# Kernel optimization log

Measured on AMD Instinct MI355X. Metric: run time of the kernel, lower is better.

## Reference

```python
import jax, jax.numpy as jnp
import numpy as np

ALPHA = 0.9   # synaptic decay
BETA = 0.8    # membrane decay
THRESH = 1.0  # snntorch default threshold, reset_mechanism='subtract'
DIMS = [7200, 3600, 1800, 900, 450]
B, T, IN_DIM, K = 128, 16, 14400, 25


def setup_inputs() -> dict:
    key = jax.random.key(0)
    ks = jax.random.split(key, 24)
    inp = {}
    inp["x"] = jax.random.normal(ks[0], (B, T, IN_DIM), jnp.float32)
    prev = IN_DIM
    for i, d in enumerate(DIMS):
        inp[f"w{i}"] = jax.random.normal(ks[1 + i], (d, K), jnp.float32) * (2.0 / K) ** 0.5
        inp[f"b{i}"] = jax.random.normal(ks[7 + i], (d,), jnp.float32) * 0.01
        inp[f"knn{i}"] = jax.random.randint(ks[13 + i], (d, K), 0, prev)
        prev = d
    inp["fc_w"] = jax.random.normal(ks[20], (2, DIMS[-1]), jnp.float32) * 0.05
    inp["fc_b"] = jax.random.normal(ks[21], (2,), jnp.float32) * 0.01
    return inp


def _forward(x, ws, bs, knns, fc_w, fc_b):
    n_layer = len(DIMS)

    def lif(inp, syn, mem):
        # snntorch Synaptic, reset_mechanism='subtract': reset computed from
        # the PREVIOUS membrane potential and detached from the graph.
        reset = jax.lax.stop_gradient((mem > THRESH).astype(inp.dtype))
        syn = ALPHA * syn + inp
        mem = BETA * mem + syn - reset * THRESH
        return syn, mem

    def step(carry, xt):
        syns, mems = carry
        h = xt  # (B, prev_dim)
        new_syns, new_mems = [], []
        for i in range(n_layer):
            g = jnp.take(h, knns[i], axis=1)                 # (B, d_i, K) KNN gather
            pre = jnp.einsum('bdk,dk->bd', g, ws[i]) + bs[i]  # weighted sum over K
            syn, mem = lif(pre, syns[i], mems[i])
            new_syns.append(syn)
            new_mems.append(mem)
            h = mem  # module propagates membrane potential to next layer
        angle = h @ fc_w.T + fc_b  # (B, 2)
        return (tuple(new_syns), tuple(new_mems)), angle

    bsz = x.shape[0]
    syns0 = tuple(jnp.zeros((bsz, d), x.dtype) for d in DIMS)
    mems0 = tuple(jnp.zeros((bsz, d), x.dtype) for d in DIMS)
    _, angles = jax.lax.scan(step, (syns0, mems0), jnp.transpose(x, (1, 0, 2)))
    return angles[-1]  # only the final timestep's angle is returned


def reference(x, w0, w1, w2, w3, w4, b0, b1, b2, b3, b4,
              knn0, knn1, knn2, knn3, knn4, fc_w, fc_b):
    return _forward(x, (w0, w1, w2, w3, w4), (b0, b1, b2, b3, b4),
                    (knn0, knn1, knn2, knn3, knn4), fc_w, fc_b)
```

## Files before the change

kernel.cpp:

```cpp
#include <hip/hip_runtime.h>

#define ALPHA 0.9f
#define BETA  0.8f
#define K     25
#define B     128
#define T     16
#define IN_DIM 14400
#define NSL   8
#define SW    16
#define CF    96
#define NCH   150

using u16 = unsigned short;

static __device__ __forceinline__ u16 f2bf(float f) {
  union { float f; unsigned u; } c; c.f = f;
  const unsigned r = c.u + 0x7FFFu + ((c.u >> 16) & 1u);
  return (u16)(r >> 16);
}
static __device__ __forceinline__ float bf2f(u16 h) {
  union { unsigned u; float f; } c; c.u = ((unsigned)h) << 16;
  return c.f;
}

__global__ __launch_bounds__(256, 4) void transpose_pair_pinned(
    const float* __restrict__ x, u16* __restrict__ xTh, int t0, int slots) {
  __shared__ float lds[CF][33];
  const int e    = blockIdx.x & 7;
  const int slot = blockIdx.x >> 3;
  const int tid  = threadIdx.x;
  const int rid  = tid >> 3;
  const int fq   = tid & 7;
  const int tpar = rid >> 4;
  const int bl   = rid & 15;
  const int b    = e * 16 + bl;

  const int ntiles = 4 * NCH;
  for (int ti = slot; ti < ntiles; ti += slots) {
    const int tp = ti / NCH;
    const int ch = ti - tp * NCH;
    const int i0 = ch * CF;
    const int t  = t0 + tp * 2 + tpar;
    const float* xr = x + ((size_t)b * T + t) * IN_DIM + i0;
#pragma unroll
    for (int pf = 0; pf < CF / 32; ++pf) {
      const float4 v = *(const float4*)&xr[pf * 32 + fq * 4];
      lds[pf * 32 + fq * 4 + 0][rid] = v.x;
      lds[pf * 32 + fq * 4 + 1][rid] = v.y;
      lds[pf * 32 + fq * 4 + 2][rid] = v.z;
      lds[pf * 32 + fq * 4 + 3][rid] = v.w;
    }
    __syncthreads();
#pragma unroll
    for (int wp = 0; wp < CF / 32; ++wp) {
      const int f = wp * 32 + rid;
      ushort4 ov;
      ov.x = f2bf(lds[f][fq * 4 + 0]);
      ov.y = f2bf(lds[f][fq * 4 + 1]);
      ov.z = f2bf(lds[f][fq * 4 + 2]);
      ov.w = f2bf(lds[f][fq * 4 + 3]);
      *(ushort4*)&xTh[(((size_t)tp * NSL + e) * IN_DIM + (i0 + f)) * 32 +
                      fq * 4] = ov;
    }
    __syncthreads();
  }
}

template <int NTP, int NPASS>
__global__ __launch_bounds__(256, 4) void lcn_pair_bf(
    const u16* __restrict__ hsrc, const float* __restrict__ w,
    const float* __restrict__ bias, const int* __restrict__ knn,
    u16* __restrict__ memout, float* __restrict__ state,
    int dim, int dprev, int nblk, int load_state, int save_state) {
  const int e    = blockIdx.x & 7;
  const int blk  = blockIdx.x >> 3;
  const int nl   = threadIdx.x >> 3;
  const int l8   = threadIdx.x & 7;
  const int half = l8 >> 2;
  const int bq   = (l8 & 3) * 4;

#pragma unroll 1
  for (int p = 0; p < NPASS; ++p) {
    const int dd = (blk + p * nblk) * 32 + nl;
    const bool act = dd < dim;
    const int d = act ? dd : dim - 1;

    int   idx[K];
    float wr[K];
#pragma unroll
    for (int k = 0; k < K; ++k) {
      idx[k] = knn[d * K + k] * 32 + half * SW + bq;
      wr[k]  = w[d * K + k];
    }
    const float bi = bias[d];

    float4 s = make_float4(0.f, 0.f, 0.f, 0.f);
    float4 m = make_float4(0.f, 0.f, 0.f, 0.f);
    if (load_state) {
      const size_t so = ((size_t)e * dim + d) * SW + bq;
      s = *(const float4*)&state[so];
      m = *(const float4*)&state[(size_t)NSL * dim * SW + so];
    }

    for (int tp = 0; tp < NTP; ++tp) {
      const u16* hp = hsrc + ((size_t)tp * NSL + e) * dprev * 32;
      ushort4 hv[13], hw[12];
#pragma unroll
      for (int j = 0; j < 13; ++j)
        hv[j] = *(const ushort4*)&hp[idx[j]];
#pragma unroll
      for (int j = 0; j < 12; ++j)
        hw[j] = *(const ushort4*)&hp[idx[13 + j]];
      float4 a0 = make_float4(bi, bi, bi, bi);
      float4 a1 = make_float4(0.f, 0.f, 0.f, 0.f);
#pragma unroll
      for (int j = 0; j < 13; ++j) {
        const float wk = wr[j];
        if (j & 1) {
          a1.x = fmaf(wk, bf2f(hv[j].x), a1.x);
          a1.y = fmaf(wk, bf2f(hv[j].y), a1.y);
          a1.z = fmaf(wk, bf2f(hv[j].z), a1.z);
          a1.w = fmaf(wk, bf2f(hv[j].w), a1.w);
        } else {
          a0.x = fmaf(wk, bf2f(hv[j].x), a0.x);
          a0.y = fmaf(wk, bf2f(hv[j].y), a0.y);
          a0.z = fmaf(wk, bf2f(hv[j].z), a0.z);
          a0.w = fmaf(wk, bf2f(hv[j].w), a0.w);
        }
      }
#pragma unroll
      for (int j = 0; j < 12; ++j) {
        const float wk = wr[13 + j];
        if (j & 1) {
          a1.x = fmaf(wk, bf2f(hw[j].x), a1.x);
          a1.y = fmaf(wk, bf2f(hw[j].y), a1.y);
          a1.z = fmaf(wk, bf2f(hw[j].z), a1.z);
          a1.w = fmaf(wk, bf2f(hw[j].w), a1.w);
        } else {
          a0.x = fmaf(wk, bf2f(hw[j].x), a0.x);
          a0.y = fmaf(wk, bf2f(hw[j].y), a0.y);
          a0.z = fmaf(wk, bf2f(hw[j].z), a0.z);
          a0.w = fmaf(wk, bf2f(hw[j].w), a0.w);
        }
      }
      float4 acc;
      acc.x = a0.x + a1.x;
      acc.y = a0.y + a1.y;
      acc.z = a0.z + a1.z;
      acc.w = a0.w + a1.w;
      float4 oth;
      oth.x = __shfl_xor(acc.x, 4, 64);
      oth.y = __shfl_xor(acc.y, 4, 64);
      oth.z = __shfl_xor(acc.z, 4, 64);
      oth.w = __shfl_xor(acc.w, 4, 64);
      const float4 pre0 = half ? oth : acc;
      const float4 pre1 = half ? acc : oth;
      s.x = ALPHA * s.x + pre0.x;
      s.y = ALPHA * s.y + pre0.y;
      s.z = ALPHA * s.z + pre0.z;
      s.w = ALPHA * s.w + pre0.w;
      float4 meven;
      meven.x = BETA * m.x + s.x - ((m.x > 1.0f) ? 1.0f : 0.0f);
      meven.y = BETA * m.y + s.y - ((m.y > 1.0f) ? 1.0f : 0.0f);
      meven.z = BETA * m.z + s.z - ((m.z > 1.0f) ? 1.0f : 0.0f);
      meven.w = BETA * m.w + s.w - ((m.w > 1.0f) ? 1.0f : 0.0f);
      s.x = ALPHA * s.x + pre1.x;
      s.y = ALPHA * s.y + pre1.y;
      s.z = ALPHA * s.z + pre1.z;
      s.w = ALPHA * s.w + pre1.w;
      m.x = BETA * meven.x + s.x - ((meven.x > 1.0f) ? 1.0f : 0.0f);
      m.y = BETA * meven.y + s.y - ((meven.y > 1.0f) ? 1.0f : 0.0f);
      m.z = BETA * meven.z + s.z - ((meven.z > 1.0f) ? 1.0f : 0.0f);
      m.w = BETA * meven.w + s.w - ((meven.w > 1.0f) ? 1.0f : 0.0f);
      if (act) {
        const float4 wv = half ? m : meven;
        ushort4 ov;
        ov.x = f2bf(wv.x);
        ov.y = f2bf(wv.y);
        ov.z = f2bf(wv.z);
        ov.w = f2bf(wv.w);
        *(ushort4*)&memout[(((size_t)tp * NSL + e) * dim + d) * 32 +
                           half * SW + bq] = ov;
      }
    }

    if (save_state && act && half == 0) {
      const size_t so = ((size_t)e * dim + d) * SW + bq;
      *(float4*)&state[so] = s;
      *(float4*)&state[(size_t)NSL * dim * SW + so] = m;
    }
  }
}

__global__ __launch_bounds__(128) void fc_kernel(
    const u16* __restrict__ mem4, const float* __restrict__ fc_w,
    const float* __restrict__ fc_b, float* __restrict__ out) {
  const int b  = threadIdx.x;
  const int e  = b >> 4;
  const int bl = b & 15;
  float a0 = fc_b[0], a1 = fc_b[1];
  const u16* base = mem4 + ((size_t)7 * NSL + e) * 450 * 32;
  for (int d = 0; d < 450; ++d) {
    const float h = bf2f(base[(size_t)d * 32 + SW + bl]);
    a0 += fc_w[d] * h;
    a1 += fc_w[450 + d] * h;
  }
  out[b * 2 + 0] = a0;
  out[b * 2 + 1] = a1;
}

extern "C" void kernel_launch(void* const* d_in, const int* in_sizes, int n_in,
                              void* d_out, int out_size, void* d_ws,
                              size_t ws_size, hipStream_t stream) {
  (void)in_sizes; (void)n_in; (void)out_size; (void)ws_size;
  const float* x = (const float*)d_in[0];
  const float* w[5];
  const float* bias[5];
  const int* knn[5];
  for (int i = 0; i < 5; ++i) {
    w[i]    = (const float*)d_in[1 + 3 * i];
    bias[i] = (const float*)d_in[2 + 3 * i];
    knn[i]  = (const int*)d_in[3 + 3 * i];
  }
  const float* fc_w = (const float*)d_in[16];
  const float* fc_b = (const float*)d_in[17];
  float* out = (float*)d_out;

  static const int DIMS[5] = {7200, 3600, 1800, 900, 450};

  u16* A  = (u16*)d_ws;
  u16* XB = A + 14745600;
  float* S = (float*)(XB + 14745600);

  u16* mem0 = A;
  u16* mem1 = XB;
  u16* mem2 = A;
  u16* mem3 = XB + 7372800;
  u16* mem4 = A;

  for (int stage = 0; stage < 2; ++stage) {
    const int t0 = stage * 8;
    transpose_pair_pinned<<<128 * NSL, 256, 0, stream>>>(x, XB, t0, 128);
    lcn_pair_bf<4, 2><<<113 * NSL, 256, 0, stream>>>(
        XB, w[0], bias[0], knn[0], mem0 + (size_t)stage * 7372800, S,
        DIMS[0], IN_DIM, 113, stage, stage == 0);
  }

  static const int NBLK[5] = {113, 113, 57, 29, 15};
  const u16* src = mem0;
  u16* dsts[4] = {mem1, mem2, mem3, mem4};
  for (int i = 1; i < 5; ++i) {
    lcn_pair_bf<8, 1><<<NBLK[i] * NSL, 256, 0, stream>>>(
        src, w[i], bias[i], knn[i], dsts[i - 1], nullptr, DIMS[i],
        DIMS[i - 1], NBLK[i], 0, 0);
    src = dsts[i - 1];
  }

  fc_kernel<<<1, 128, 0, stream>>>(mem4, fc_w, fc_b, out);
}
```

Baseline: 336.0 us.

## Use 16-byte gathers with 64 neurons per block and LDS-staged indices

Rewrites the LCN layer kernel so each thread handles 8 batch lanes with ushort8 (16-byte) gathers instead of 4 lanes with 8-byte loads. Each block now covers 64 neurons, and the KNN indices and weights are staged in shared memory instead of per-thread registers. The gather loads are software-pipelined in groups of five. The aim is fewer, wider gather transactions and lower register pressure, at the cost of fewer blocks for the small layers (as few as 64) and LDS reads inside the inner loop.

```diff
diff --git a/kernel.cpp b/kernel.cpp
--- a/kernel.cpp
+++ b/kernel.cpp
@@ -12,6 +12,7 @@
 #define NCH   150
 
 using u16 = unsigned short;
+typedef __attribute__((ext_vector_type(8))) unsigned short ushort8;
 
 static __device__ __forceinline__ u16 f2bf(float f) {
   union { float f; unsigned u; } c; c.f = f;
@@ -66,129 +67,144 @@
   }
 }
 
-template <int NTP, int NPASS>
-__global__ __launch_bounds__(256, 4) void lcn_pair_bf(
+template <int NTP>
+__global__ __launch_bounds__(256, 4) void lcn16(
     const u16* __restrict__ hsrc, const float* __restrict__ w,
     const float* __restrict__ bias, const int* __restrict__ knn,
     u16* __restrict__ memout, float* __restrict__ state,
-    int dim, int dprev, int nblk, int load_state, int save_state) {
+    int dim, int dprev, int load_state, int save_state) {
+  __shared__ int   sidx[64][K];
+  __shared__ float swr[64][K];
+
   const int e    = blockIdx.x & 7;
   const int blk  = blockIdx.x >> 3;
-  const int nl   = threadIdx.x >> 3;
-  const int l8   = threadIdx.x & 7;
-  const int half = l8 >> 2;
-  const int bq   = (l8 & 3) * 4;
-
-#pragma unroll 1
-  for (int p = 0; p < NPASS; ++p) {
-    const int dd = (blk + p * nblk) * 32 + nl;
-    const bool act = dd < dim;
-    const int d = act ? dd : dim - 1;
-
-    int   idx[K];
-    float wr[K];
-#pragma unroll
-    for (int k = 0; k < K; ++k) {
-      idx[k] = knn[d * K + k] * 32 + half * SW + bq;
-      wr[k]  = w[d * K + k];
+  const int nl   = threadIdx.x >> 2;
+  const int l4   = threadIdx.x & 3;
+  const int half = l4 >> 1;
+  const int oct  = l4 & 1;
+  const int lofs = half * SW + oct * 8;
+
+  const int dd  = blk * 64 + nl;
+  const bool act = dd < dim;
+  const int d   = act ? dd : dim - 1;
+
+  for (int i = threadIdx.x; i < 64 * K; i += 256) {
+    const int n = i / K, k = i - n * K;
+    int dn = blk * 64 + n;
+    if (dn >= dim) dn = dim - 1;
+    sidx[n][k] = knn[dn * K + k] * 32;
+    swr[n][k]  = w[dn * K + k];
+  }
+  __syncthreads();
+
+  const float bi = bias[d];
+
+  float4 sL = make_float4(0.f, 0.f, 0.f, 0.f), sH = sL, mL = sL, mH = sL;
+  if (load_state) {
+    const size_t so = ((size_t)e * dim + d) * SW + oct * 8;
+    sL = *(const float4*)&state[so];
+    sH = *(const float4*)&state[so + 4];
+    mL = *(const float4*)&state[(size_t)NSL * dim * SW + so];
+    mH = *(const float4*)&state[(size_t)NSL * dim * SW + so + 4];
+  }
+
+#define FMA8(wk, hv)                                 \
+  do {                                               \
+    aL.x = fmaf(wk, bf2f((hv)[0]), aL.x);            \
+    aL.y = fmaf(wk, bf2f((hv)[1]), aL.y);            \
+    aL.z = fmaf(wk, bf2f((hv)[2]), aL.z);            \
+    aL.w = fmaf(wk, bf2f((hv)[3]), aL.w);            \
+    aH.x = fmaf(wk, bf2f((hv)[4]), aH.x);            \
+    aH.y = fmaf(wk, bf2f((hv)[5]), aH.y);            \
+    aH.z = fmaf(wk, bf2f((hv)[6]), aH.z);            \
+    aH.w = fmaf(wk, bf2f((hv)[7]), aH.w);            \
+  } while (0)
+
+  for (int tp = 0; tp < NTP; ++tp) {
+    const u16* hp = hsrc + ((size_t)tp * NSL + e) * dprev * 32;
+    ushort8 ha[5], hb[5];
+#pragma unroll
+    for (int j = 0; j < 5; ++j) ha[j] = *(const ushort8*)&hp[sidx[nl][j] + lofs];
+#pragma unroll
+    for (int j = 0; j < 5; ++j) hb[j] = *(const ushort8*)&hp[sidx[nl][5 + j] + lofs];
+    float4 aL = make_float4(bi, bi, bi, bi);
+    float4 aH = make_float4(bi, bi, bi, bi);
+#pragma unroll
+    for (int j = 0; j < 5; ++j) FMA8(swr[nl][j], ha[j]);
+#pragma unroll
+    for (int j = 0; j < 5; ++j) ha[j] = *(const ushort8*)&hp[sidx[nl][10 + j] + lofs];
+#pragma unroll
+    for (int j = 0; j < 5; ++j) FMA8(swr[nl][5 + j], hb[j]);
+#pragma unroll
+    for (int j = 0; j < 5; ++j) hb[j] = *(const ushort8*)&hp[sidx[nl][15 + j] + lofs];
+#pragma unroll
+    for (int j = 0; j < 5; ++j) FMA8(swr[nl][10 + j], ha[j]);
+#pragma unroll
+    for (int j = 0; j < 5; ++j) ha[j] = *(const ushort8*)&hp[sidx[nl][20 + j] + lofs];
+#pragma unroll
+    for (int j = 0; j < 5; ++j) FMA8(swr[nl][15 + j], hb[j]);
+#pragma unroll
+    for (int j = 0; j < 5; ++j) FMA8(swr[nl][20 + j], ha[j]);
+
+    float4 oL, oH;
+    oL.x = __shfl_xor(aL.x, 2, 64);
+    oL.y = __shfl_xor(aL.y, 2, 64);
+    oL.z = __shfl_xor(aL.z, 2, 64);
+    oL.w = __shfl_xor(aL.w, 2, 64);
+    oH.x = __shfl_xor(aH.x, 2, 64);
+    oH.y = __shfl_xor(aH.y, 2, 64);
+    oH.z = __shfl_xor(aH.z, 2, 64);
+    oH.w = __shfl_xor(aH.w, 2, 64);
+    const float4 p0L = half ? oL : aL;
+    const float4 p0H = half ? oH : aH;
+    const float4 p1L = half ? aL : oL;
+    const float4 p1H = half ? aH : oH;
+
+    sL.x = ALPHA * sL.x + p0L.x;  sL.y = ALPHA * sL.y + p0L.y;
+    sL.z = ALPHA * sL.z + p0L.z;  sL.w = ALPHA * sL.w + p0L.w;
+    sH.x = ALPHA * sH.x + p0H.x;  sH.y = ALPHA * sH.y + p0H.y;
+    sH.z = ALPHA * sH.z + p0H.z;  sH.w = ALPHA * sH.w + p0H.w;
+    float4 meL, meH;
+    meL.x = BETA * mL.x + sL.x - ((mL.x > 1.0f) ? 1.0f : 0.0f);
+    meL.y = BETA * mL.y + sL.y - ((mL.y > 1.0f) ? 1.0f : 0.0f);
+    meL.z = BETA * mL.z + sL.z - ((mL.z > 1.0f) ? 1.0f : 0.0f);
+    meL.w = BETA * mL.w + sL.w - ((mL.w > 1.0f) ? 1.0f : 0.0f);
+    meH.x = BETA * mH.x + sH.x - ((mH.x > 1.0f) ? 1.0f : 0.0f);
+    meH.y = BETA * mH.y + sH.y - ((mH.y > 1.0f) ? 1.0f : 0.0f);
+    meH.z = BETA * mH.z + sH.z - ((mH.z > 1.0f) ? 1.0f : 0.0f);
+    meH.w = BETA * mH.w + sH.w - ((mH.w > 1.0f) ? 1.0f : 0.0f);
+    sL.x = ALPHA * sL.x + p1L.x;  sL.y = ALPHA * sL.y + p1L.y;
+    sL.z = ALPHA * sL.z + p1L.z;  sL.w = ALPHA * sL.w + p1L.w;
+    sH.x = ALPHA * sH.x + p1H.x;  sH.y = ALPHA * sH.y + p1H.y;
+    sH.z = ALPHA * sH.z + p1H.z;  sH.w = ALPHA * sH.w + p1H.w;
+    mL.x = BETA * meL.x + sL.x - ((meL.x > 1.0f) ? 1.0f : 0.0f);
+    mL.y = BETA * meL.y + sL.y - ((meL.y > 1.0f) ? 1.0f : 0.0f);
+    mL.z = BETA * meL.z + sL.z - ((meL.z > 1.0f) ? 1.0f : 0.0f);
+    mL.w = BETA * meL.w + sL.w - ((meL.w > 1.0f) ? 1.0f : 0.0f);
+    mH.x = BETA * meH.x + sH.x - ((meH.x > 1.0f) ? 1.0f : 0.0f);
+    mH.y = BETA * meH.y + sH.y - ((meH.y > 1.0f) ? 1.0f : 0.0f);
+    mH.z = BETA * meH.z + sH.z - ((meH.z > 1.0f) ? 1.0f : 0.0f);
+    mH.w = BETA * meH.w + sH.w - ((meH.w > 1.0f) ? 1.0f : 0.0f);
+
+    if (act) {
+      const float4 wvL = half ? mL : meL;
+      const float4 wvH = half ? mH : meH;
+      ushort8 ov;
+      ov[0] = f2bf(wvL.x); ov[1] = f2bf(wvL.y);
+      ov[2] = f2bf(wvL.z); ov[3] = f2bf(wvL.w);
+      ov[4] = f2bf(wvH.x); ov[5] = f2bf(wvH.y);
+      ov[6] = f2bf(wvH.z); ov[7] = f2bf(wvH.w);
+      *(ushort8*)&memout[(((size_t)tp * NSL + e) * dim + d) * 32 + lofs] = ov;
     }
-    const float bi = bias[d];
-
-    float4 s = make_float4(0.f, 0.f, 0.f, 0.f);
-    float4 m = make_float4(0.f, 0.f, 0.f, 0.f);
-    if (load_state) {
-      const size_t so = ((size_t)e * dim + d) * SW + bq;
-      s = *(const float4*)&state[so];
-      m = *(const float4*)&state[(size_t)NSL * dim * SW + so];
-    }
-
-    for (int tp = 0; tp < NTP; ++tp) {
-      const u16* hp = hsrc + ((size_t)tp * NSL + e) * dprev * 32;
-      ushort4 hv[13], hw[12];
-#pragma unroll
-      for (int j = 0; j < 13; ++j)
-        hv[j] = *(const ushort4*)&hp[idx[j]];
-#pragma unroll
-      for (int j = 0; j < 12; ++j)
-        hw[j] = *(const ushort4*)&hp[idx[13 + j]];
-      float4 a0 = make_float4(bi, bi, bi, bi);
-      float4 a1 = make_float4(0.f, 0.f, 0.f, 0.f);
-#pragma unroll
-      for (int j = 0; j < 13; ++j) {
-        const float wk = wr[j];
-        if (j & 1) {
-          a1.x = fmaf(wk, bf2f(hv[j].x), a1.x);
-          a1.y = fmaf(wk, bf2f(hv[j].y), a1.y);
-          a1.z = fmaf(wk, bf2f(hv[j].z), a1.z);
-          a1.w = fmaf(wk, bf2f(hv[j].w), a1.w);
-        } else {
-          a0.x = fmaf(wk, bf2f(hv[j].x), a0.x);
-          a0.y = fmaf(wk, bf2f(hv[j].y), a0.y);
-          a0.z = fmaf(wk, bf2f(hv[j].z), a0.z);
-          a0.w = fmaf(wk, bf2f(hv[j].w), a0.w);
-        }
-      }
-#pragma unroll
-      for (int j = 0; j < 12; ++j) {
-        const float wk = wr[13 + j];
-        if (j & 1) {
-          a1.x = fmaf(wk, bf2f(hw[j].x), a1.x);
-          a1.y = fmaf(wk, bf2f(hw[j].y), a1.y);
-          a1.z = fmaf(wk, bf2f(hw[j].z), a1.z);
-          a1.w = fmaf(wk, bf2f(hw[j].w), a1.w);
-        } else {
-          a0.x = fmaf(wk, bf2f(hw[j].x), a0.x);
-          a0.y = fmaf(wk, bf2f(hw[j].y), a0.y);
-          a0.z = fmaf(wk, bf2f(hw[j].z), a0.z);
-          a0.w = fmaf(wk, bf2f(hw[j].w), a0.w);
-        }
-      }
-      float4 acc;
-      acc.x = a0.x + a1.x;
-      acc.y = a0.y + a1.y;
-      acc.z = a0.z + a1.z;
-      acc.w = a0.w + a1.w;
-      float4 oth;
-      oth.x = __shfl_xor(acc.x, 4, 64);
-      oth.y = __shfl_xor(acc.y, 4, 64);
-      oth.z = __shfl_xor(acc.z, 4, 64);
-      oth.w = __shfl_xor(acc.w, 4, 64);
-      const float4 pre0 = half ? oth : acc;
-      const float4 pre1 = half ? acc : oth;
-      s.x = ALPHA * s.x + pre0.x;
-      s.y = ALPHA * s.y + pre0.y;
-      s.z = ALPHA * s.z + pre0.z;
-      s.w = ALPHA * s.w + pre0.w;
-      float4 meven;
-      meven.x = BETA * m.x + s.x - ((m.x > 1.0f) ? 1.0f : 0.0f);
-      meven.y = BETA * m.y + s.y - ((m.y > 1.0f) ? 1.0f : 0.0f);
-      meven.z = BETA * m.z + s.z - ((m.z > 1.0f) ? 1.0f : 0.0f);
-      meven.w = BETA * m.w + s.w - ((m.w > 1.0f) ? 1.0f : 0.0f);
-      s.x = ALPHA * s.x + pre1.x;
-      s.y = ALPHA * s.y + pre1.y;
-      s.z = ALPHA * s.z + pre1.z;
-      s.w = ALPHA * s.w + pre1.w;
-      m.x = BETA * meven.x + s.x - ((meven.x > 1.0f) ? 1.0f : 0.0f);
-      m.y = BETA * meven.y + s.y - ((meven.y > 1.0f) ? 1.0f : 0.0f);
-      m.z = BETA * meven.z + s.z - ((meven.z > 1.0f) ? 1.0f : 0.0f);
-      m.w = BETA * meven.w + s.w - ((meven.w > 1.0f) ? 1.0f : 0.0f);
-      if (act) {
-        const float4 wv = half ? m : meven;
-        ushort4 ov;
-        ov.x = f2bf(wv.x);
-        ov.y = f2bf(wv.y);
-        ov.z = f2bf(wv.z);
-        ov.w = f2bf(wv.w);
-        *(ushort4*)&memout[(((size_t)tp * NSL + e) * dim + d) * 32 +
-                           half * SW + bq] = ov;
-      }
-    }
-
-    if (save_state && act && half == 0) {
-      const size_t so = ((size_t)e * dim + d) * SW + bq;
-      *(float4*)&state[so] = s;
-      *(float4*)&state[(size_t)NSL * dim * SW + so] = m;
-    }
+  }
+#undef FMA8
+
+  if (save_state && act && half == 0) {
+    const size_t so = ((size_t)e * dim + d) * SW + oct * 8;
+    *(float4*)&state[so] = sL;
+    *(float4*)&state[so + 4] = sH;
+    *(float4*)&state[(size_t)NSL * dim * SW + so] = mL;
+    *(float4*)&state[(size_t)NSL * dim * SW + so + 4] = mH;
   }
 }
 
@@ -226,8 +242,6 @@
   const float* fc_b = (const float*)d_in[17];
   float* out = (float*)d_out;
 
-  static const int DIMS[5] = {7200, 3600, 1800, 900, 450};
-
   u16* A  = (u16*)d_ws;
   u16* XB = A + 14745600;
   float* S = (float*)(XB + 14745600);
@@ -241,20 +255,19 @@
   for (int stage = 0; stage < 2; ++stage) {
     const int t0 = stage * 8;
     transpose_pair_pinned<<<128 * NSL, 256, 0, stream>>>(x, XB, t0, 128);
-    lcn_pair_bf<4, 2><<<113 * NSL, 256, 0, stream>>>(
+    lcn16<4><<<113 * NSL, 256, 0, stream>>>(
         XB, w[0], bias[0], knn[0], mem0 + (size_t)stage * 7372800, S,
-        DIMS[0], IN_DIM, 113, stage, stage == 0);
-  }
-
-  static const int NBLK[5] = {113, 113, 57, 29, 15};
-  const u16* src = mem0;
-  u16* dsts[4] = {mem1, mem2, mem3, mem4};
-  for (int i = 1; i < 5; ++i) {
-    lcn_pair_bf<8, 1><<<NBLK[i] * NSL, 256, 0, stream>>>(
-        src, w[i], bias[i], knn[i], dsts[i - 1], nullptr, DIMS[i],
-        DIMS[i - 1], NBLK[i], 0, 0);
-    src = dsts[i - 1];
-  }
+        7200, IN_DIM, stage, stage == 0);
+  }
+
+  lcn16<8><<<57 * NSL, 256, 0, stream>>>(mem0, w[1], bias[1], knn[1], mem1,
+                                         nullptr, 3600, 7200, 0, 0);
+  lcn16<8><<<29 * NSL, 256, 0, stream>>>(mem1, w[2], bias[2], knn[2], mem2,
+                                         nullptr, 1800, 3600, 0, 0);
+  lcn16<8><<<15 * NSL, 256, 0, stream>>>(mem2, w[3], bias[3], knn[3], mem3,
+                                         nullptr, 900, 1800, 0, 0);
+  lcn16<8><<<8 * NSL, 256, 0, stream>>>(mem3, w[4], bias[4], knn[4], mem4,
+                                        nullptr, 450, 900, 0, 0);
 
   fc_kernel<<<1, 128, 0, stream>>>(mem4, fc_w, fc_b, out);
 }
```

After: 585.6 us. +74.3%, slower.
